# Kernel tuning notes

Measured on AMD Instinct MI355X. Metric: run time of the kernel, lower is better.

The kernel has to match this reference:

```python
import jax, jax.numpy as jnp
import numpy as np

N_PANO, N_FP = 50000, 10000
D_IN, D_FP, HID, OUT = 128, 64, 128, 64
E_PP, E_PF = 800000, 50000


def _gat(x_src, x_dst, src, dst, Ws, Wd, a_s, a_d, b, n_dst):
    # PyG GATConv (heads=1, add_self_loops=False, bipartite lin_src/lin_dst)
    hs = x_src @ Ws                      # [Ns, C]
    hd = x_dst @ Wd                      # [Nd, C]
    es = hs @ a_s                        # [Ns]
    ed = hd @ a_d                        # [Nd]
    e = jax.nn.leaky_relu(es[src] + ed[dst], negative_slope=0.2)  # [E]
    m = jax.ops.segment_max(e, dst, num_segments=n_dst)
    ex = jnp.exp(e - m[dst])
    den = jax.ops.segment_sum(ex, dst, num_segments=n_dst)
    alpha = ex / den[dst]                # segment softmax over incoming edges
    out = jax.ops.segment_sum(hs[src] * alpha[:, None], dst, num_segments=n_dst)
    return out + b


def setup_inputs() -> dict:
    key = jax.random.key(0)
    ks = jax.random.split(key, 32)
    s_in = 1.0 / np.sqrt(D_IN)
    s_hid = 1.0 / np.sqrt(HID)
    s_fp = 1.0 / np.sqrt(D_FP)
    inp = {
        "x_pano": jax.random.normal(ks[0], (N_PANO, D_IN), jnp.float32),
        "x_fp": jax.random.normal(ks[1], (N_FP, D_FP), jnp.float32),
        # layer 0 (in = D_IN)
        "Ws0": jax.random.normal(ks[2], (D_IN, HID)) * s_in,
        "Wd0": jax.random.normal(ks[3], (D_IN, HID)) * s_in,
        "as0": jax.random.normal(ks[4], (HID,)) * 0.1,
        "ad0": jax.random.normal(ks[5], (HID,)) * 0.1,
        "b0": jnp.zeros((HID,), jnp.float32),
        "Lw0": jax.random.normal(ks[6], (D_IN, HID)) * s_in,
        "Lb0": jnp.zeros((HID,), jnp.float32),
        # layer 1 (in = HID)
        "Ws1": jax.random.normal(ks[7], (HID, HID)) * s_hid,
        "Wd1": jax.random.normal(ks[8], (HID, HID)) * s_hid,
        "as1": jax.random.normal(ks[9], (HID,)) * 0.1,
        "ad1": jax.random.normal(ks[10], (HID,)) * 0.1,
        "b1": jnp.zeros((HID,), jnp.float32),
        "Lw1": jax.random.normal(ks[11], (HID, HID)) * s_hid,
        "Lb1": jnp.zeros((HID,), jnp.float32),
        # translate conv pano -> footprint
        "Wts": jax.random.normal(ks[12], (HID, OUT)) * s_hid,
        "Wtd": jax.random.normal(ks[13], (D_FP, OUT)) * s_fp,
        "ats": jax.random.normal(ks[14], (OUT,)) * 0.1,
        "atd": jax.random.normal(ks[15], (OUT,)) * 0.1,
        "bt": jnp.zeros((OUT,), jnp.float32),
        "edge_pp": jax.random.randint(ks[16], (2, E_PP), 0, N_PANO),
        "edge_pf_src": jax.random.randint(ks[17], (E_PF,), 0, N_PANO),
        "edge_pf_dst": jax.random.randint(ks[18], (E_PF,), 0, N_FP),
    }
    return inp


def reference(x_pano, x_fp, Ws0, Wd0, as0, ad0, b0, Lw0, Lb0,
              Ws1, Wd1, as1, ad1, b1, Lw1, Lb1,
              Wts, Wtd, ats, atd, bt,
              edge_pp, edge_pf_src, edge_pf_dst):
    src, dst = edge_pp[0], edge_pp[1]
    layer_params = [(Ws0, Wd0, as0, ad0, b0, Lw0, Lb0),
                    (Ws1, Wd1, as1, ad1, b1, Lw1, Lb1)]
    h = x_pano
    for (Ws, Wd, a_s, a_d, b, Lw, Lb) in layer_params:
        conv = _gat(h, h, src, dst, Ws, Wd, a_s, a_d, b, N_PANO)
        h = jax.nn.relu(conv + h @ Lw + Lb)
    # HeteroConv with single relation + aggr='sum' == the bipartite conv output
    out_fp = _gat(h, x_fp, edge_pf_src, edge_pf_dst, Wts, Wtd, ats, atd, bt, N_FP)
    return out_fp
```

## Files before the change

### kernel.cpp

```cpp
#include <hip/hip_runtime.h>
#include <hip/hip_bf16.h>
#include <math.h>

#define N_PANO 50000
#define N_FP   10000
#define N_UNI  60000
#define HID    128
#define OUT_C  64
#define E_PP   800000
#define E_PF   50000
#define E_UNI  850000
#define NBKT   235
#define EPB    16384
#define NT_CNT 52
#define NT_GEMM 391

typedef unsigned short ushort_t;
typedef unsigned int uint_t;
typedef __attribute__((ext_vector_type(8))) short short8;
typedef __attribute__((ext_vector_type(4))) float f32x4;

static inline int cdiv(int a, int b) { return (a + b - 1) / b; }

__device__ inline ushort_t f2bf(float x) {
    __hip_bfloat16 h = __float2bfloat16(x);
    return *reinterpret_cast<ushort_t*>(&h);
}
__device__ inline float bfu2f(ushort_t u) {
    return __uint_as_float(((uint_t)u) << 16);
}
__device__ inline float bflo(uint_t u) { return __uint_as_float((u & 0xffffu) << 16); }
__device__ inline float bfhi(uint_t u) { return __uint_as_float(u & 0xffff0000u); }
__device__ inline f32x4 mfma16(short8 a, short8 b, f32x4 c) {
    return __builtin_amdgcn_mfma_f32_16x16x32_bf16(a, b, c, 0, 0, 0);
}

__global__ __launch_bounds__(256) void csr_count_prep(
        const int* __restrict__ pp_dst, const int* __restrict__ pf_dst,
        int* __restrict__ pcnt,
        const float* __restrict__ Ws0, const float* __restrict__ Lw0,
        const float* __restrict__ Ws1, const float* __restrict__ Lw1,
        const float* __restrict__ Wts,
        const float* __restrict__ Wd0, const float* __restrict__ ad0,
        const float* __restrict__ Wd1, const float* __restrict__ ad1,
        const float* __restrict__ Wtd, const float* __restrict__ atd,
        ushort_t* s0, ushort_t* l0, ushort_t* s1, ushort_t* l1, ushort_t* ts,
        float* wed0, float* wed1, float* wedt) {
    __shared__ int hist[NBKT];
    const int tile = blockIdx.x, tid = threadIdx.x;
    if (tile < NT_CNT) {
        for (int t = tid; t < NBKT; t += 256) hist[t] = 0;
        __syncthreads();
        const int e0 = tile * EPB;
        #pragma unroll 8
        for (int u = 0; u < 64; ++u) {
            int e = e0 + u * 256 + tid;
            int d = -1;
            if (e < E_PP) d = pp_dst[e];
            else if (e < E_UNI) d = N_PANO + pf_dst[e - E_PP];
            if (d >= 0) atomicAdd(&hist[d >> 8], 1);
        }
        __syncthreads();
        for (int t = tid; t < NBKT; t += 256) pcnt[tile * NBKT + t] = hist[t];
    } else if (tile < NT_CNT + 288) {
        int i = (tile - NT_CNT) * 256 + tid;
        const float* W; ushort_t* oh;
        int d, NIc, Cc;
        if (i < 65536) {
            int m = i >> 14; d = i & 16383;
            W = (m == 0) ? Ws0 : (m == 1) ? Lw0 : (m == 2) ? Ws1 : Lw1;
            oh = (m == 0) ? s0 : (m == 1) ? l0 : (m == 2) ? s1 : l1;
            NIc = 8; Cc = 128;
        } else if (i < 73728) {
            d = i - 65536; W = Wts; oh = ts;
            NIc = 4; Cc = 64;
        } else return;
        int j = d & 7, l = (d >> 3) & 63;
        int kcl = (d >> 9) & 1;
        int ni = (d >> 10) & (NIc - 1);
        int p = d >> (10 + (NIc == 8 ? 3 : 2));
        int kc = p * 2 + kcl;
        int n = ni * 16 + (l & 15);
        int k = kc * 32 + (l >> 4) * 8 + j;
        oh[d] = f2bf(W[k * Cc + n]);
    } else {
        int r = (tile - NT_CNT - 288) * 4 + (tid >> 6);
        int lane = tid & 63;
        const float* W; const float* a; float* o; int rr, C;
        if (r < 128)      { W = Wd0; a = ad0; o = wed0; rr = r;       C = 128; }
        else if (r < 256) { W = Wd1; a = ad1; o = wed1; rr = r - 128; C = 128; }
        else if (r < 320) { W = Wtd; a = atd; o = wedt; rr = r - 256; C = 64;  }
        else return;
        float s = 0.f;
        for (int j = lane; j < C; j += 64) s += W[rr * C + j] * a[j];
        #pragma unroll
        for (int off = 32; off; off >>= 1) s += __shfl_down(s, off, 64);
        if (lane == 0) o[rr] = s;
    }
}

template <int CN, bool DUAL, bool FP32IN>
__device__ void gemm_body(int tile, char* smem,
                          const float* __restrict__ Xf, const ushort_t* __restrict__ Xh,
                          const ushort_t* __restrict__ W1, const ushort_t* __restrict__ W2,
                          ushort_t* __restrict__ Y1, ushort_t* __restrict__ Y2,
                          const float* __restrict__ avec, float* __restrict__ evec,
                          const float* __restrict__ wed, float* __restrict__ edv, int N) {
    constexpr int NI = CN / 16;
    constexpr int SLAB = NI * 1024;
    ushort_t* Bsh = (ushort_t*)smem;
    const int tid = threadIdx.x;
    const int w = tid >> 6, l = tid & 63;
    const int col = l & 15, q = l >> 4;
    const int row0 = tile * 128 + w * 32;
    f32x4 acc1[2][NI];
    f32x4 acc2[2][DUAL ? NI : 1];
    #pragma unroll
    for (int m = 0; m < 2; ++m)
        #pragma unroll
        for (int ni = 0; ni < NI; ++ni)
            #pragma unroll
            for (int r = 0; r < 4; ++r) acc1[m][ni][r] = 0.f;
    if (DUAL) {
        #pragma unroll
        for (int m = 0; m < 2; ++m)
            #pragma unroll
            for (int ni = 0; ni < NI; ++ni)
                #pragma unroll
                for (int r = 0; r < 4; ++r) acc2[m][ni][r] = 0.f;
    }
    float ped[2] = {0.f, 0.f};

    #pragma unroll
    for (int p = 0; p < 2; ++p) {
        if (p) __syncthreads();
        {
            const uint4* src1 = (const uint4*)W1 + p * (SLAB / 8);
            uint4* dst1 = (uint4*)&Bsh[0];
            #pragma unroll
            for (int f = tid; f < SLAB / 8; f += 256) dst1[f] = src1[f];
            if (DUAL) {
                const uint4* src2 = (const uint4*)W2 + p * (SLAB / 8);
                uint4* dst2 = (uint4*)&Bsh[SLAB];
                #pragma unroll
                for (int f = tid; f < SLAB / 8; f += 256) dst2[f] = src2[f];
            }
        }
        __syncthreads();
        #pragma unroll
        for (int kcl = 0; kcl < 2; ++kcl) {
            const int kc = p * 2 + kcl;
            const int k0 = kc * 32 + q * 8;
            short8 Ah[2];
            #pragma unroll
            for (int m = 0; m < 2; ++m) {
                const int arow = row0 + m * 16 + col;
                if (FP32IN) {
                    float xv[8];
                    if (arow < N) {
                        float4 a0 = *(const float4*)&Xf[(size_t)arow * 128 + k0];
                        float4 a1 = *(const float4*)&Xf[(size_t)arow * 128 + k0 + 4];
                        xv[0] = a0.x; xv[1] = a0.y; xv[2] = a0.z; xv[3] = a0.w;
                        xv[4] = a1.x; xv[5] = a1.y; xv[6] = a1.z; xv[7] = a1.w;
                    } else {
                        #pragma unroll
                        for (int j = 0; j < 8; ++j) xv[j] = 0.f;
                    }
                    #pragma unroll
                    for (int j = 0; j < 8; ++j) Ah[m][j] = (short)f2bf(xv[j]);
                    if (wed) {
                        float4 w0 = *(const float4*)&wed[k0];
                        float4 w1 = *(const float4*)&wed[k0 + 4];
                        ped[m] += xv[0] * w0.x + xv[1] * w0.y + xv[2] * w0.z + xv[3] * w0.w
                                + xv[4] * w1.x + xv[5] * w1.y + xv[6] * w1.z + xv[7] * w1.w;
                    }
                } else {
                    if (arow < N) {
                        Ah[m] = *(const short8*)&Xh[(size_t)arow * 128 + k0];
                    } else {
                        #pragma unroll
                        for (int j = 0; j < 8; ++j) Ah[m][j] = 0;
                    }
                    if (wed) {
                        float4 w0 = *(const float4*)&wed[k0];
                        float4 w1 = *(const float4*)&wed[k0 + 4];
                        float wv[8] = {w0.x, w0.y, w0.z, w0.w, w1.x, w1.y, w1.z, w1.w};
                        #pragma unroll
                        for (int j = 0; j < 8; ++j)
                            ped[m] += bfu2f((ushort_t)Ah[m][j]) * wv[j];
                    }
                }
            }
            #pragma unroll
            for (int ni = 0; ni < NI; ++ni) {
                const int lb = ((ni * 2 + kcl) * 64 + l) * 8;
                short8 B1 = *(const short8*)&Bsh[lb];
                #pragma unroll
                for (int m = 0; m < 2; ++m) acc1[m][ni] = mfma16(Ah[m], B1, acc1[m][ni]);
                if (DUAL) {
                    short8 B2 = *(const short8*)&Bsh[SLAB + lb];
                    #pragma unroll
                    for (int m = 0; m < 2; ++m) acc2[m][ni] = mfma16(Ah[m], B2, acc2[m][ni]);
                }
            }
        }
    }

    #pragma unroll
    for (int m = 0; m < 2; ++m) {
        #pragma unroll
        for (int ni = 0; ni < NI; ++ni) {
            #pragma unroll
            for (int r = 0; r < 4; ++r) {
                int mrow = row0 + m * 16 + q * 4 + r;
                if (mrow < N) {
                    Y1[(size_t)mrow * CN + ni * 16 + col] = f2bf(acc1[m][ni][r]);
                    if (DUAL) Y2[(size_t)mrow * CN + ni * 16 + col] = f2bf(acc2[m][ni][r]);
                }
            }
        }
    }
    float av[NI];
    #pragma unroll
    for (int ni = 0; ni < NI; ++ni) av[ni] = avec[ni * 16 + col];
    #pragma unroll
    for (int m = 0; m < 2; ++m) {
        #pragma unroll
        for (int r = 0; r < 4; ++r) {
            float pp = 0.f;
            #pragma unroll
            for (int ni = 0; ni < NI; ++ni) pp += acc1[m][ni][r] * av[ni];
            pp += __shfl_xor(pp, 1, 64);
            pp += __shfl_xor(pp, 2, 64);
            pp += __shfl_xor(pp, 4, 64);
            pp += __shfl_xor(pp, 8, 64);
            int mrow = row0 + m * 16 + q * 4 + r;
            if (col == 0 && mrow < N) evec[mrow] = pp;
        }
    }
    if (wed) {
        #pragma unroll
        for (int m = 0; m < 2; ++m) {
            ped[m] += __shfl_xor(ped[m], 16, 64);
            ped[m] += __shfl_xor(ped[m], 32, 64);
            int arow = row0 + m * 16 + col;
            if (q == 0 && arow < N) edv[arow] = ped[m];
        }
    }
}

__device__ void scatter_body(int tile, char* smem,
                             const int* __restrict__ pp_src, const int* __restrict__ pp_dst,
                             const int* __restrict__ pf_src, const int* __restrict__ pf_dst,
                             const int* __restrict__ pcnt, int* __restrict__ bbase_out,
                             int2* __restrict__ tmp) {
    int* base2 = (int*)smem;
    int* cur   = base2 + NBKT;
    int* wsum  = cur + NBKT;
    const int tid = threadIdx.x, lane = tid & 63, wv = tid >> 6;
    int rowsum = 0, myprefix = 0;
    if (tid < NBKT) {
        const int* pb = pcnt + tid;
        int t = 0;
        for (; t + 8 <= NT_CNT; t += 8) {
            int c0 = pb[(t + 0) * NBKT], c1 = pb[(t + 1) * NBKT];
            int c2 = pb[(t + 2) * NBKT], c3 = pb[(t + 3) * NBKT];
            int c4 = pb[(t + 4) * NBKT], c5 = pb[(t + 5) * NBKT];
            int c6 = pb[(t + 6) * NBKT], c7 = pb[(t + 7) * NBKT];
            rowsum += c0 + c1 + c2 + c3 + c4 + c5 + c6 + c7;
            myprefix += ((t + 0 < tile) ? c0 : 0) + ((t + 1 < tile) ? c1 : 0)
                      + ((t + 2 < tile) ? c2 : 0) + ((t + 3 < tile) ? c3 : 0)
                      + ((t + 4 < tile) ? c4 : 0) + ((t + 5 < tile) ? c5 : 0)
                      + ((t + 6 < tile) ? c6 : 0) + ((t + 7 < tile) ? c7 : 0);
        }
        for (; t < NT_CNT; ++t) {
            int c = pb[t * NBKT];
            rowsum += c;
            if (t < tile) myprefix += c;
        }
    }
    int v = (tid < NBKT) ? rowsum : 0;
    int incl = v;
    #pragma unroll
    for (int off = 1; off < 64; off <<= 1) {
        int t = __shfl_up(incl, off, 64);
        if (lane >= off) incl += t;
    }
    if (lane == 63) wsum[wv] = incl;
    __syncthreads();
    if (tid == 0) {
        int run = 0;
        #pragma unroll
        for (int w = 0; w < 4; ++w) { int t = wsum[w]; wsum[w] = run; run += t; }
    }
    __syncthreads();
    int bexcl = wsum[wv] + incl - v;
    if (tid < NBKT) {
        base2[tid] = bexcl + myprefix;
        cur[tid] = 0;
        if (tile == 0) bbase_out[tid] = bexcl;
    }
    if (tile == 0 && tid == 0) bbase_out[NBKT] = E_UNI;
    __syncthreads();
    const int e0 = tile * EPB;
    #pragma unroll 8
    for (int u = 0; u < 64; ++u) {
        int e = e0 + u * 256 + tid;
        int d = -1, s = 0;
        if (e < E_PP)       { d = pp_dst[e];                 s = pp_src[e]; }
        else if (e < E_UNI) { d = N_PANO + pf_dst[e - E_PP]; s = pf_src[e - E_PP]; }
        if (d >= 0) {
            int b = d >> 8;
            int p = base2[b] + atomicAdd(&cur[b], 1);
            tmp[p] = make_int2(s, d);
        }
    }
}

__global__ __launch_bounds__(256, 2) void scatter_gemm0(
        const int* __restrict__ pp_src, const int* __restrict__ pp_dst,
        const int* __restrict__ pf_src, const int* __restrict__ pf_dst,
        const int* __restrict__ pcnt, int* __restrict__ bbase_out, int2* __restrict__ tmp,
        const float* __restrict__ x_pano,
        const ushort_t* __restrict__ s0, const ushort_t* __restrict__ l0,
        ushort_t* __restrict__ hsb, ushort_t* __restrict__ linb,
        const float* __restrict__ as0, float* __restrict__ es,
        const float* __restrict__ wed0, float* __restrict__ ed) {
    __shared__ __align__(16) char smem[32768];
    if (blockIdx.x < NT_CNT)
        scatter_body(blockIdx.x, smem, pp_src, pp_dst, pf_src, pf_dst, pcnt, bbase_out, tmp);
    else
        gemm_body<128, true, true>(blockIdx.x - NT_CNT, smem, x_pano, nullptr, s0, l0,
                                   hsb, linb, as0, es, wed0, ed, N_PANO);
}

template <int CN, bool DUAL, bool FP32IN>
__global__ __launch_bounds__(256, 2) void gemm_mfma(const float* __restrict__ Xf,
                                                 const ushort_t* __restrict__ Xh,
                                                 const ushort_t* __restrict__ W1, const ushort_t* __restrict__ W2,
                                                 ushort_t* __restrict__ Y1, ushort_t* __restrict__ Y2,
                                                 const float* __restrict__ avec, float* __restrict__ evec,
                                                 const float* __restrict__ wed, float* __restrict__ edv,
                                                 int N) {
    __shared__ __align__(16) char smem[(DUAL ? 2 : 1) * (CN / 16) * 2048];
    gemm_body<CN, DUAL, FP32IN>(blockIdx.x, smem, Xf, Xh, W1, W2, Y1, Y2, avec, evec, wed, edv, N);
}

__global__ __launch_bounds__(256) void csr_sort(const int2* __restrict__ tmp,
                                                const int* __restrict__ bbase,
                                                int* __restrict__ ptr, int* __restrict__ col) {
    __shared__ int hist[256];
    __shared__ int wsum[4];
    const int b = blockIdx.x, tid = threadIdx.x, lane = tid & 63, wv = tid >> 6;
    const int B0 = bbase[b], B1 = bbase[b + 1];
    hist[tid] = 0;
    __syncthreads();
    for (int e = B0 + tid; e < B1; e += 256) atomicAdd(&hist[tmp[e].y & 255], 1);
    __syncthreads();
    int v = hist[tid];
    int incl = v;
    #pragma unroll
    for (int off = 1; off < 64; off <<= 1) {
        int t = __shfl_up(incl, off, 64);
        if (lane >= off) incl += t;
    }
    if (lane == 63) wsum[wv] = incl;
    __syncthreads();
    if (tid == 0) {
        int run = 0;
        #pragma unroll
        for (int w = 0; w < 4; ++w) { int t = wsum[w]; wsum[w] = run; run += t; }
    }
    __syncthreads();
    int excl = wsum[wv] + incl - v;
    int dg = b * 256 + tid;
    if (dg < N_UNI) ptr[dg] = B0 + excl;
    if (b == NBKT - 1 && tid == 0) ptr[N_UNI] = E_UNI;
    hist[tid] = excl;
    __syncthreads();
    for (int e = B0 + tid; e < B1; e += 256) {
        int2 ed2 = tmp[e];
        int p = B0 + atomicAdd(&hist[ed2.y & 255], 1);
        col[p] = ed2.x;
    }
}

__global__ __launch_bounds__(256) void agg_pano7(const int* __restrict__ ptr, const int* __restrict__ col,
                                                 const float* __restrict__ es, const float* __restrict__ ed,
                                                 const ushort_t* __restrict__ hsb, const ushort_t* __restrict__ linb,
                                                 const float* __restrict__ b, const float* __restrict__ Lb,
                                                 uint_t* __restrict__ hh, int N) {
    int lane = threadIdx.x & 63, wid = threadIdx.x >> 6;
    int nodeA = blockIdx.x * 8 + wid * 2;
    if (nodeA >= N) return;
    int nodeB = nodeA + 1;
    bool hasB = nodeB < N;
    int begA = ptr[nodeA], endA = ptr[nodeA + 1];
    int endB = hasB ? ptr[nodeB + 1] : endA;
    int begB = endA;
    float ednA = ed[nodeA];
    float ednB = hasB ? ed[nodeB] : 0.f;
    const int half = lane >> 5, hl = lane & 31;
    float aA0 = 0.f, aA1 = 0.f, aA2 = 0.f, aA3 = 0.f, dA = 0.f;
    float aB0 = 0.f, aB1 = 0.f, aB2 = 0.f, aB3 = 0.f, dB = 0.f;
    int baseA = begA, baseB = begB;
    while (baseA < endA || baseB < endB) {
        int mA = endA - baseA; mA = mA < 0 ? 0 : (mA > 64 ? 64 : mA);
        int mB = endB - baseB; mB = mB < 0 ? 0 : (mB > 64 ? 64 : mB);
        int sA = 0, sB = 0;
        float wA = 0.f, wB = 0.f;
        if (lane < mA) {
            sA = col[baseA + lane];
            float e = es[sA] + ednA;
            e = fmaxf(e, 0.2f * e);
            wA = __expf(e);
        }
        if (lane < mB) {
            sB = col[baseB + lane];
            float e = es[sB] + ednB;
            e = fmaxf(e, 0.2f * e);
            wB = __expf(e);
        }
        dA += wA; dB += wB;
        {
            int mp = (mA + 1) & ~1;
            int t = 0;
            for (; t + 8 <= mp; t += 8) {
                int i0 = t + half, i1 = t + 2 + half, i2 = t + 4 + half, i3 = t + 6 + half;
                int s0 = __shfl(sA, i0, 64), s1 = __shfl(sA, i1, 64);
                int s2 = __shfl(sA, i2, 64), s3 = __shfl(sA, i3, 64);
                float w0 = __shfl(wA, i0, 64), w1 = __shfl(wA, i1, 64);
                float w2 = __shfl(wA, i2, 64), w3 = __shfl(wA, i3, 64);
                uint2 h0 = *(const uint2*)&hsb[(size_t)s0 * 128 + hl * 4];
                uint2 h1 = *(const uint2*)&hsb[(size_t)s1 * 128 + hl * 4];
                uint2 h2 = *(const uint2*)&hsb[(size_t)s2 * 128 + hl * 4];
                uint2 h3 = *(const uint2*)&hsb[(size_t)s3 * 128 + hl * 4];
                aA0 += w0 * bflo(h0.x) + w1 * bflo(h1.x) + w2 * bflo(h2.x) + w3 * bflo(h3.x);
                aA1 += w0 * bfhi(h0.x) + w1 * bfhi(h1.x) + w2 * bfhi(h2.x) + w3 * bfhi(h3.x);
                aA2 += w0 * bflo(h0.y) + w1 * bflo(h1.y) + w2 * bflo(h2.y) + w3 * bflo(h3.y);
                aA3 += w0 * bfhi(h0.y) + w1 * bfhi(h1.y) + w2 * bfhi(h2.y) + w3 * bfhi(h3.y);
            }
            for (; t < mp; t += 2) {
                int i0 = t + half;
                int s0 = __shfl(sA, i0, 64);
                float w0 = __shfl(wA, i0, 64);
                uint2 h0 = *(const uint2*)&hsb[(size_t)s0 * 128 + hl * 4];
                aA0 += w0 * bflo(h0.x);
                aA1 += w0 * bfhi(h0.x);
                aA2 += w0 * bflo(h0.y);
                aA3 += w0 * bfhi(h0.y);
            }
        }
        {
            int mp = (mB + 1) & ~1;
            int t = 0;
            for (; t + 8 <= mp; t += 8) {
                int i0 = t + half, i1 = t + 2 + half, i2 = t + 4 + half, i3 = t + 6 + half;
                int s0 = __shfl(sB, i0, 64), s1 = __shfl(sB, i1, 64);
                int s2 = __shfl(sB, i2, 64), s3 = __shfl(sB, i3, 64);
                float w0 = __shfl(wB, i0, 64), w1 = __shfl(wB, i1, 64);
                float w2 = __shfl(wB, i2, 64), w3 = __shfl(wB, i3, 64);
                uint2 h0 = *(const uint2*)&hsb[(size_t)s0 * 128 + hl * 4];
                uint2 h1 = *(const uint2*)&hsb[(size_t)s1 * 128 + hl * 4];
                uint2 h2 = *(const uint2*)&hsb[(size_t)s2 * 128 + hl * 4];
                uint2 h3 = *(const uint2*)&hsb[(size_t)s3 * 128 + hl * 4];
                aB0 += w0 * bflo(h0.x) + w1 * bflo(h1.x) + w2 * bflo(h2.x) + w3 * bflo(h3.x);
                aB1 += w0 * bfhi(h0.x) + w1 * bfhi(h1.x) + w2 * bfhi(h2.x) + w3 * bfhi(h3.x);
                aB2 += w0 * bflo(h0.y) + w1 * bflo(h1.y) + w2 * bflo(h2.y) + w3 * bflo(h3.y);
                aB3 += w0 * bfhi(h0.y) + w1 * bfhi(h1.y) + w2 * bfhi(h2.y) + w3 * bfhi(h3.y);
            }
            for (; t < mp; t += 2) {
                int i0 = t + half;
                int s0 = __shfl(sB, i0, 64);
                float w0 = __shfl(wB, i0, 64);
                uint2 h0 = *(const uint2*)&hsb[(size_t)s0 * 128 + hl * 4];
                aB0 += w0 * bflo(h0.x);
                aB1 += w0 * bfhi(h0.x);
                aB2 += w0 * bflo(h0.y);
                aB3 += w0 * bfhi(h0.y);
            }
        }
        baseA += 64; baseB += 64;
    }
    aA0 += __shfl_xor(aA0, 32, 64); aA1 += __shfl_xor(aA1, 32, 64);
    aA2 += __shfl_xor(aA2, 32, 64); aA3 += __shfl_xor(aA3, 32, 64);
    aB0 += __shfl_xor(aB0, 32, 64); aB1 += __shfl_xor(aB1, 32, 64);
    aB2 += __shfl_xor(aB2, 32, 64); aB3 += __shfl_xor(aB3, 32, 64);
    #pragma unroll
    for (int off = 1; off < 64; off <<= 1) dA += __shfl_xor(dA, off, 64);
    #pragma unroll
    for (int off = 1; off < 64; off <<= 1) dB += __shfl_xor(dB, off, 64);
    float invA = (endA > begA) ? (1.f / dA) : 0.f;
    float invB = (endB > begB) ? (1.f / dB) : 0.f;
    int node = half ? nodeB : nodeA;
    if (half == 0 || hasB) {
        float v0 = half ? aB0 : aA0, v1 = half ? aB1 : aA1;
        float v2 = half ? aB2 : aA2, v3 = half ? aB3 : aA3;
        float inv = half ? invB : invA;
        uint2 lv = *(const uint2*)&linb[(size_t)node * 128 + hl * 4];
        float4 bb = *(const float4*)&b[hl * 4];
        float4 lb4 = *(const float4*)&Lb[hl * 4];
        float o0 = fmaxf(v0 * inv + bb.x + bflo(lv.x) + lb4.x, 0.f);
        float o1 = fmaxf(v1 * inv + bb.y + bfhi(lv.x) + lb4.y, 0.f);
        float o2 = fmaxf(v2 * inv + bb.z + bflo(lv.y) + lb4.z, 0.f);
        float o3 = fmaxf(v3 * inv + bb.w + bfhi(lv.y) + lb4.w, 0.f);
        uint2 ov;
        ov.x = (uint_t)f2bf(o0) | ((uint_t)f2bf(o1) << 16);
        ov.y = (uint_t)f2bf(o2) | ((uint_t)f2bf(o3) << 16);
        *(uint2*)&hh[(size_t)node * 64 + hl * 2] = ov;
    }
}

__global__ __launch_bounds__(256) void agg_fp5(const int* __restrict__ ptr, const int* __restrict__ col,
                                               const float* __restrict__ es, const float* __restrict__ x_fp,
                                               const float* __restrict__ wedt,
                                               const ushort_t* __restrict__ hsb, const float* __restrict__ bt,
                                               float* __restrict__ out, int N) {
    int lane = threadIdx.x & 63, wid = threadIdx.x >> 6;
    int node = blockIdx.x * 4 + wid;
    if (node >= N) return;
    int beg = ptr[node], end = ptr[node + 1];
    float edn = x_fp[(size_t)node * 64 + lane] * wedt[lane];
    #pragma unroll
    for (int off = 1; off < 64; off <<= 1) edn += __shfl_xor(edn, off, 64);
    float acc = 0.f, denp = 0.f;
    for (int base = beg; base < end; base += 64) {
        int m = min(64, end - base);
        int s = 0;
        float wgt = 0.f;
        if (lane < m) {
            s = col[base + lane];
            float e = es[s] + edn;
            e = fmaxf(e, 0.2f * e);
            wgt = __expf(e);
        }
        denp += wgt;
        int u = 0;
        for (; u + 4 <= m; u += 4) {
            int s0 = __shfl(s, u, 64), s1 = __shfl(s, u + 1, 64);
            int s2 = __shfl(s, u + 2, 64), s3 = __shfl(s, u + 3, 64);
            float w0 = __shfl(wgt, u, 64), w1 = __shfl(wgt, u + 1, 64);
            float w2 = __shfl(wgt, u + 2, 64), w3 = __shfl(wgt, u + 3, 64);
            float h0 = bfu2f(hsb[(size_t)s0 * 64 + lane]);
            float h1 = bfu2f(hsb[(size_t)s1 * 64 + lane]);
            float h2 = bfu2f(hsb[(size_t)s2 * 64 + lane]);
            float h3 = bfu2f(hsb[(size_t)s3 * 64 + lane]);
            acc += w0 * h0 + w1 * h1 + w2 * h2 + w3 * h3;
        }
        for (; u < m; ++u) {
            int su = __shfl(s, u, 64);
            float wu = __shfl(wgt, u, 64);
            acc += wu * bfu2f(hsb[(size_t)su * 64 + lane]);
        }
    }
    float den = denp;
    #pragma unroll
    for (int off = 1; off < 64; off <<= 1) den += __shfl_xor(den, off, 64);
    float inv = (end > beg) ? (1.f / den) : 0.f;
    out[(size_t)node * 64 + lane] = acc * inv + bt[lane];
}

extern "C" void kernel_launch(void* const* d_in, const int* in_sizes, int n_in,
                              void* d_out, int out_size, void* d_ws, size_t ws_size,
                              hipStream_t stream) {
    const float* x_pano = (const float*)d_in[0];
    const float* x_fp   = (const float*)d_in[1];
    const float* Ws0 = (const float*)d_in[2];
    const float* Wd0 = (const float*)d_in[3];
    const float* as0 = (const float*)d_in[4];
    const float* ad0 = (const float*)d_in[5];
    const float* b0  = (const float*)d_in[6];
    const float* Lw0 = (const float*)d_in[7];
    const float* Lb0 = (const float*)d_in[8];
    const float* Ws1 = (const float*)d_in[9];
    const float* Wd1 = (const float*)d_in[10];
    const float* as1 = (const float*)d_in[11];
    const float* ad1 = (const float*)d_in[12];
    const float* b1  = (const float*)d_in[13];
    const float* Lw1 = (const float*)d_in[14];
    const float* Lb1 = (const float*)d_in[15];
    const float* Wts = (const float*)d_in[16];
    const float* Wtd = (const float*)d_in[17];
    const float* ats = (const float*)d_in[18];
    const float* atd = (const float*)d_in[19];
    const float* bt  = (const float*)d_in[20];
    const int* pp_src = (const int*)d_in[21];
    const int* pp_dst = (const int*)d_in[21] + E_PP;
    const int* pf_src = (const int*)d_in[22];
    const int* pf_dst = (const int*)d_in[23];
    float* out = (float*)d_out;

    char* wsp = (char*)d_ws;
    size_t off = 0;
    auto alloc = [&](size_t bytes) -> char* {
        char* p = wsp + off;
        off += (bytes + 255) & ~(size_t)255;
        return p;
    };
    ushort_t* hsb  = (ushort_t*)alloc(sizeof(ushort_t) * N_PANO * HID);
    ushort_t* linb = (ushort_t*)alloc(sizeof(ushort_t) * N_PANO * HID);
    uint_t* hh     = (uint_t*)alloc(sizeof(uint_t) * N_PANO * 64);
    ushort_t* hstb = (ushort_t*)alloc(sizeof(ushort_t) * N_PANO * OUT_C);
    int2* tmp_e    = (int2*)alloc(sizeof(int2) * E_UNI);
    float* es   = (float*)alloc(sizeof(float) * N_PANO);
    float* ed   = (float*)alloc(sizeof(float) * N_PANO);
    float* wed0 = (float*)alloc(sizeof(float) * HID);
    float* wed1 = (float*)alloc(sizeof(float) * HID);
    float* wedt = (float*)alloc(sizeof(float) * OUT_C);
    ushort_t* s0 = (ushort_t*)alloc(sizeof(ushort_t) * 128 * 128);
    ushort_t* l0 = (ushort_t*)alloc(sizeof(ushort_t) * 128 * 128);
    ushort_t* s1 = (ushort_t*)alloc(sizeof(ushort_t) * 128 * 128);
    ushort_t* l1 = (ushort_t*)alloc(sizeof(ushort_t) * 128 * 128);
    ushort_t* ts = (ushort_t*)alloc(sizeof(ushort_t) * 64 * 128);
    int* pcnt  = (int*)alloc(sizeof(int) * NBKT * NT_CNT);
    int* bbase = (int*)alloc(sizeof(int) * (NBKT + 1));
    int* P     = (int*)alloc(sizeof(int) * (N_UNI + 1));
    int* col_u = (int*)alloc(sizeof(int) * E_UNI);

    csr_count_prep<<<NT_CNT + 288 + 80, 256, 0, stream>>>(
        pp_dst, pf_dst, pcnt, Ws0, Lw0, Ws1, Lw1, Wts,
        Wd0, ad0, Wd1, ad1, Wtd, atd, s0, l0, s1, l1, ts, wed0, wed1, wedt);

    scatter_gemm0<<<NT_CNT + NT_GEMM, 256, 0, stream>>>(
        pp_src, pp_dst, pf_src, pf_dst, pcnt, bbase, tmp_e,
        x_pano, s0, l0, hsb, linb, as0, es, wed0, ed);

    csr_sort<<<NBKT, 256, 0, stream>>>(tmp_e, bbase, P, col_u);

    agg_pano7<<<cdiv(N_PANO, 8), 256, 0, stream>>>(P, col_u, es, ed, hsb, linb, b0, Lb0, hh, N_PANO);

    gemm_mfma<128, true, false><<<NT_GEMM, 256, 0, stream>>>(
        nullptr, (const ushort_t*)hh, s1, l1, hsb, linb, as1, es, wed1, ed, N_PANO);

    agg_pano7<<<cdiv(N_PANO, 8), 256, 0, stream>>>(P, col_u, es, ed, hsb, linb, b1, Lb1, hh, N_PANO);

    gemm_mfma<64, false, false><<<NT_GEMM, 256, 0, stream>>>(
        nullptr, (const ushort_t*)hh, ts, nullptr, hstb, nullptr, ats, es, nullptr, nullptr, N_PANO);

    agg_fp5<<<cdiv(N_FP, 4), 256, 0, stream>>>(P + N_PANO, col_u, es, x_fp, wedt, hstb, bt, out, N_FP);
}
```

Before: 290.9 us.

## Read GEMM weights directly from global memory and shrink CSR edge tiles

The GEMM body no longer stages weight slabs into shared memory with barriers. Each lane now loads its B fragments straight from global memory, relying on the small weights staying in cache, and LDS use drops so occupancy can rise. Separately, the CSR count and scatter phases use 4096 edges per tile instead of 16384, which gives four times as many blocks for more parallelism. The trade-off is more per-lane global or L2 weight traffic in the GEMM and a larger per-tile count array to prefix-sum.

```diff
diff --git a/kernel.cpp b/kernel.cpp
--- a/kernel.cpp
+++ b/kernel.cpp
@@ -11,8 +11,8 @@
 #define E_PF   50000
 #define E_UNI  850000
 #define NBKT   235
-#define EPB    16384
-#define NT_CNT 52
+#define EPB    4096
+#define NT_CNT 208
 #define NT_GEMM 391
 
 typedef unsigned short ushort_t;
@@ -52,8 +52,8 @@
         for (int t = tid; t < NBKT; t += 256) hist[t] = 0;
         __syncthreads();
         const int e0 = tile * EPB;
-        #pragma unroll 8
-        for (int u = 0; u < 64; ++u) {
+        #pragma unroll
+        for (int u = 0; u < 16; ++u) {
             int e = e0 + u * 256 + tid;
             int d = -1;
             if (e < E_PP) d = pp_dst[e];
@@ -100,7 +100,7 @@
 }
 
 template <int CN, bool DUAL, bool FP32IN>
-__device__ void gemm_body(int tile, char* smem,
+__device__ void gemm_body(int tile,
                           const float* __restrict__ Xf, const ushort_t* __restrict__ Xh,
                           const ushort_t* __restrict__ W1, const ushort_t* __restrict__ W2,
                           ushort_t* __restrict__ Y1, ushort_t* __restrict__ Y2,
@@ -108,7 +108,6 @@
                           const float* __restrict__ wed, float* __restrict__ edv, int N) {
     constexpr int NI = CN / 16;
     constexpr int SLAB = NI * 1024;
-    ushort_t* Bsh = (ushort_t*)smem;
     const int tid = threadIdx.x;
     const int w = tid >> 6, l = tid & 63;
     const int col = l & 15, q = l >> 4;
@@ -133,20 +132,6 @@
 
     #pragma unroll
     for (int p = 0; p < 2; ++p) {
-        if (p) __syncthreads();
-        {
-            const uint4* src1 = (const uint4*)W1 + p * (SLAB / 8);
-            uint4* dst1 = (uint4*)&Bsh[0];
-            #pragma unroll
-            for (int f = tid; f < SLAB / 8; f += 256) dst1[f] = src1[f];
-            if (DUAL) {
-                const uint4* src2 = (const uint4*)W2 + p * (SLAB / 8);
-                uint4* dst2 = (uint4*)&Bsh[SLAB];
-                #pragma unroll
-                for (int f = tid; f < SLAB / 8; f += 256) dst2[f] = src2[f];
-            }
-        }
-        __syncthreads();
         #pragma unroll
         for (int kcl = 0; kcl < 2; ++kcl) {
             const int kc = p * 2 + kcl;
@@ -193,12 +178,12 @@
             }
             #pragma unroll
             for (int ni = 0; ni < NI; ++ni) {
-                const int lb = ((ni * 2 + kcl) * 64 + l) * 8;
-                short8 B1 = *(const short8*)&Bsh[lb];
+                const int gb = p * SLAB + ((ni * 2 + kcl) * 64 + l) * 8;
+                short8 B1 = *(const short8*)&W1[gb];
                 #pragma unroll
                 for (int m = 0; m < 2; ++m) acc1[m][ni] = mfma16(Ah[m], B1, acc1[m][ni]);
                 if (DUAL) {
-                    short8 B2 = *(const short8*)&Bsh[SLAB + lb];
+                    short8 B2 = *(const short8*)&W2[gb];
                     #pragma unroll
                     for (int m = 0; m < 2; ++m) acc2[m][ni] = mfma16(Ah[m], B2, acc2[m][ni]);
                 }
@@ -303,8 +288,8 @@
     if (tile == 0 && tid == 0) bbase_out[NBKT] = E_UNI;
     __syncthreads();
     const int e0 = tile * EPB;
-    #pragma unroll 8
-    for (int u = 0; u < 64; ++u) {
+    #pragma unroll
+    for (int u = 0; u < 16; ++u) {
         int e = e0 + u * 256 + tid;
         int d = -1, s = 0;
         if (e < E_PP)       { d = pp_dst[e];                 s = pp_src[e]; }
@@ -326,11 +311,11 @@
         ushort_t* __restrict__ hsb, ushort_t* __restrict__ linb,
         const float* __restrict__ as0, float* __restrict__ es,
         const float* __restrict__ wed0, float* __restrict__ ed) {
-    __shared__ __align__(16) char smem[32768];
+    __shared__ __align__(16) char smem[(2 * NBKT + 4) * 4];
     if (blockIdx.x < NT_CNT)
         scatter_body(blockIdx.x, smem, pp_src, pp_dst, pf_src, pf_dst, pcnt, bbase_out, tmp);
     else
-        gemm_body<128, true, true>(blockIdx.x - NT_CNT, smem, x_pano, nullptr, s0, l0,
+        gemm_body<128, true, true>(blockIdx.x - NT_CNT, x_pano, nullptr, s0, l0,
                                    hsb, linb, as0, es, wed0, ed, N_PANO);
 }
 
@@ -342,8 +327,7 @@
                                                  const float* __restrict__ avec, float* __restrict__ evec,
                                                  const float* __restrict__ wed, float* __restrict__ edv,
                                                  int N) {
-    __shared__ __align__(16) char smem[(DUAL ? 2 : 1) * (CN / 16) * 2048];
-    gemm_body<CN, DUAL, FP32IN>(blockIdx.x, smem, Xf, Xh, W1, W2, Y1, Y2, avec, evec, wed, edv, N);
+    gemm_body<CN, DUAL, FP32IN>(blockIdx.x, Xf, Xh, W1, W2, Y1, Y2, avec, evec, wed, edv, N);
 }
 
 __global__ __launch_bounds__(256) void csr_sort(const int2* __restrict__ tmp,
```

New measurement: 268.4 us. 1.08x faster.
